# Kernel tuning notes

Measured on AMD Instinct MI355X. Metric: run time of the kernel, lower is better.

Reference implementation:

```python
import jax, jax.numpy as jnp
import numpy as np

# Mamba config (HF defaults for hidden_size=256)
VOCAB = 4096
H = 256          # hidden_size
I = 512          # intermediate_size = 2*H
N = 16           # state_size
R = 16           # time_step_rank = ceil(H/16)
K = 4            # conv_kernel
NUM_LAYERS = 4
B, L = 4, 1024
EPS = 1e-5


def _rmsnorm(x, w):
    return x * jax.lax.rsqrt(jnp.mean(x * x, axis=-1, keepdims=True) + EPS) * w


def setup_inputs() -> dict:
    key = jax.random.key(0)
    ks = jax.random.split(key, 20)
    s = 0.02
    Lyr = NUM_LAYERS
    inp = {
        'input_ids': jax.random.randint(ks[0], (B, L), 0, VOCAB),
        'lengths': jax.random.randint(ks[1], (B,), 1, L + 1),
        'embed': jax.random.normal(ks[2], (VOCAB, H)) * s,
        'norm_w': jnp.ones((Lyr, H)),
        'in_proj_w': jax.random.normal(ks[3], (Lyr, 2 * I, H)) * s,
        'conv_w': jax.random.normal(ks[4], (Lyr, I, K)) * s,
        'conv_b': jnp.zeros((Lyr, I)),
        'x_proj_w': jax.random.normal(ks[5], (Lyr, R + 2 * N, I)) * s,
        'dt_proj_w': jax.random.normal(ks[6], (Lyr, I, R)) * s,
        'dt_proj_b': jax.random.normal(ks[7], (Lyr, I)) * 0.5 - 4.0,
        'A_log': jnp.log(jnp.broadcast_to(jnp.arange(1, N + 1, dtype=jnp.float32), (Lyr, I, N))),
        'D': jnp.ones((Lyr, I)),
        'out_proj_w': jax.random.normal(ks[8], (Lyr, H, I)) * s,
        'final_norm_w': jnp.ones((H,)),
        'head_w1': jax.random.normal(ks[9], (H // 4, H)) * s,
        'head_b1': jnp.zeros((H // 4,)),
        'head_w2': jax.random.normal(ks[10], (1, H // 4)) * s,
        'head_b2': jnp.zeros((1,)),
    }
    return inp


def _mixer(x, in_proj_w, conv_w, conv_b, x_proj_w, dt_proj_w, dt_proj_b, A_log, D_, out_proj_w):
    b, l, _ = x.shape
    proj = x @ in_proj_w.T                      # (b,l,2I)
    xs, gate = proj[..., :I], proj[..., I:]
    # depthwise causal conv1d (kernel K, left pad K-1)
    xp = jnp.pad(xs, ((0, 0), (K - 1, 0), (0, 0)))
    conv = sum(xp[:, k:k + l, :] * conv_w[:, k] for k in range(K))
    xs = jax.nn.silu(conv + conv_b)             # (b,l,I)
    ssm = xs @ x_proj_w.T                       # (b,l,R+2N)
    dt_r, Bmat, Cmat = ssm[..., :R], ssm[..., R:R + N], ssm[..., R + N:]
    dt = jax.nn.softplus(dt_r @ dt_proj_w.T + dt_proj_b)   # (b,l,I)
    A = -jnp.exp(A_log)                         # (I,N)
    dA = jnp.exp(dt[..., None] * A)             # (b,l,I,N)
    dBu = (dt * xs)[..., None] * Bmat[:, :, None, :]        # (b,l,I,N)

    def step(state, inputs):
        a_t, bu_t, c_t = inputs                 # (b,I,N),(b,I,N),(b,N)
        state = a_t * state + bu_t
        y = jnp.einsum('bdn,bn->bd', state, c_t)
        return state, y

    state0 = jnp.zeros((b, I, N), dtype=x.dtype)
    _, ys = jax.lax.scan(step, state0, (dA.transpose(1, 0, 2, 3),
                                        dBu.transpose(1, 0, 2, 3),
                                        Cmat.transpose(1, 0, 2)))
    ys = ys.transpose(1, 0, 2)                  # (b,l,I)
    y = (ys + xs * D_) * jax.nn.silu(gate)
    return y @ out_proj_w.T                     # (b,l,H)


def reference(input_ids, lengths, embed, norm_w, in_proj_w, conv_w, conv_b,
              x_proj_w, dt_proj_w, dt_proj_b, A_log, D, out_proj_w,
              final_norm_w, head_w1, head_b1, head_w2, head_b2):
    h = embed[input_ids]                        # (B,L,H)
    for i in range(NUM_LAYERS):
        res = h
        x = _rmsnorm(h, norm_w[i])
        h = res + _mixer(x, in_proj_w[i], conv_w[i], conv_b[i], x_proj_w[i],
                         dt_proj_w[i], dt_proj_b[i], A_log[i], D[i], out_proj_w[i])
    h = _rmsnorm(h, final_norm_w)
    pooled = h[jnp.arange(h.shape[0]), lengths - 1]         # (B,H)
    hd = jax.nn.gelu(pooled @ head_w1.T + head_b1, approximate=False)
    out = hd @ head_w2.T + head_b2
    return out.squeeze(-1)                      # (B,)
```

## Files before the change

### kernel.cpp

```cpp
#include <hip/hip_runtime.h>
#include <hip/hip_bf16.h>

#define HDIM 256
#define IDIM 512
#define NST 16
#define KCONV 4
#define LAYERS 4
#define BATCH 4
#define LSEQ 1024
#define TOK (BATCH * LSEQ)

typedef unsigned short u16;
typedef float f32x4 __attribute__((ext_vector_type(4)));
typedef short bf16x8 __attribute__((ext_vector_type(8)));

static __device__ __forceinline__ u16 f2bf(float f) {
    __hip_bfloat16 h = __float2bfloat16(f);
    return reinterpret_cast<u16&>(h);
}
static __device__ __forceinline__ float bf2f(u16 b) {
    return __builtin_bit_cast(float, (unsigned)b << 16);
}
static __device__ __forceinline__ float bfup(uint2 u, int j) {
    unsigned w = (j < 2) ? u.x : u.y;
    unsigned bits = (j & 1) ? (w & 0xffff0000u) : (w << 16);
    return __builtin_bit_cast(float, bits);
}

#define DPP_ROW_ADD(p, CTRL)                                                   \
    p += __builtin_bit_cast(float, __builtin_amdgcn_update_dpp(                \
             0, __builtin_bit_cast(int, p), CTRL, 0xf, 0xf, false))

__global__ __launch_bounds__(256) void embed_kernel(const int* __restrict__ ids,
                                                    const float* __restrict__ embed,
                                                    float* __restrict__ h) {
    int idx = blockIdx.x * 256 + threadIdx.x;
    if (idx < TOK * HDIM) {
        int tok = idx >> 8;
        int c = idx & (HDIM - 1);
        h[idx] = embed[ids[tok] * HDIM + c];
    }
}

__global__ __launch_bounds__(256) void cvt4_bf16_kernel(const float* __restrict__ s0, u16* __restrict__ d0,
                                                        const float* __restrict__ s1, u16* __restrict__ d1,
                                                        const float* __restrict__ s2, u16* __restrict__ d2,
                                                        const float* __restrict__ s3, u16* __restrict__ d3) {
    const float* in;
    u16* out;
    int base;
    int bid = blockIdx.x;
    if (bid < 1024)      { in = s0; out = d0; base = bid; }
    else if (bid < 1536) { in = s1; out = d1; base = bid - 1024; }
    else if (bid < 1632) { in = s2; out = d2; base = bid - 1536; }
    else                 { in = s3; out = d3; base = bid - 1632; }
    int j = (base * 256 + threadIdx.x) * 4;
    float4 v = *(const float4*)&in[j];
    unsigned lo = (unsigned)f2bf(v.x) | ((unsigned)f2bf(v.y) << 16);
    unsigned hi = (unsigned)f2bf(v.z) | ((unsigned)f2bf(v.w) << 16);
    *(uint2*)&out[j] = make_uint2(lo, hi);
}

__global__ __launch_bounds__(256) void rmsnorm_kernel(const float* __restrict__ h,
                                                      const float* __restrict__ w,
                                                      u16* __restrict__ xb) {
    int wid = threadIdx.x >> 6, lane = threadIdx.x & 63;
    int tok = blockIdx.x * 4 + wid;
    float4 v = *(const float4*)&h[(size_t)tok * HDIM + lane * 4];
    float s = v.x * v.x + v.y * v.y + v.z * v.z + v.w * v.w;
    #pragma unroll
    for (int m = 32; m >= 1; m >>= 1) s += __shfl_xor(s, m, 64);
    float rstd = rsqrtf(s * (1.0f / HDIM) + 1e-5f);
    float4 wv = *(const float4*)&w[lane * 4];
    unsigned lo = (unsigned)f2bf(v.x * rstd * wv.x) | ((unsigned)f2bf(v.y * rstd * wv.y) << 16);
    unsigned hi = (unsigned)f2bf(v.z * rstd * wv.z) | ((unsigned)f2bf(v.w * rstd * wv.w) << 16);
    *(uint2*)&xb[(size_t)tok * HDIM + lane * 4] = make_uint2(lo, hi);
}

__global__ __launch_bounds__(256) void gemm_bf16_kernel(const u16* __restrict__ A,
                                                        const u16* __restrict__ W,
                                                        u16* __restrict__ C,
                                                        int M, int N, int K) {
    const int BM = 128, BK = 32;
    __shared__ __align__(16) u16 Al[BM][BK + 8];
    __shared__ __align__(16) u16 Bl[BM][BK + 8];
    int m0 = blockIdx.y * BM, n0 = blockIdx.x * BM;
    int tid = threadIdx.x;
    int lane = tid & 63;
    int wid = tid >> 6;
    int wr = wid >> 1, wc = wid & 1;
    int r = lane & 15, g = lane >> 4;

    f32x4 acc[4][4] = {};

    int srow = tid & 127;
    const u16* src = (tid < 128) ? (A + (size_t)(m0 + srow) * K)
                                 : (W + (size_t)(n0 + srow) * K);
    u16* dstrow = (tid < 128) ? &Al[srow][0] : &Bl[srow][0];

    for (int k0 = 0; k0 < K; k0 += BK) {
        uint4 v0 = *(const uint4*)(src + k0);
        uint4 v1 = *(const uint4*)(src + k0 + 8);
        uint4 v2 = *(const uint4*)(src + k0 + 16);
        uint4 v3 = *(const uint4*)(src + k0 + 24);
        __syncthreads();
        *(uint4*)(dstrow)      = v0;
        *(uint4*)(dstrow + 8)  = v1;
        *(uint4*)(dstrow + 16) = v2;
        *(uint4*)(dstrow + 24) = v3;
        __syncthreads();

        bf16x8 af[4], bfr[4];
        #pragma unroll
        for (int f = 0; f < 4; ++f) {
            af[f]  = *(const bf16x8*)&Al[wr * 64 + f * 16 + r][g * 8];
            bfr[f] = *(const bf16x8*)&Bl[wc * 64 + f * 16 + r][g * 8];
        }
        #pragma unroll
        for (int fm = 0; fm < 4; ++fm)
            #pragma unroll
            for (int fn = 0; fn < 4; ++fn)
                acc[fm][fn] = __builtin_amdgcn_mfma_f32_16x16x32_bf16(
                    af[fm], bfr[fn], acc[fm][fn], 0, 0, 0);
    }

    #pragma unroll
    for (int fm = 0; fm < 4; ++fm) {
        #pragma unroll
        for (int fn = 0; fn < 4; ++fn) {
            int col = n0 + wc * 64 + fn * 16 + r;
            #pragma unroll
            for (int v = 0; v < 4; ++v) {
                int row = m0 + wr * 64 + fm * 16 + g * 4 + v;
                C[(size_t)row * N + col] = f2bf(acc[fm][fn][v]);
            }
        }
    }
}

__global__ __launch_bounds__(256) void outproj_norm_kernel(const u16* __restrict__ Y,
                                                           const u16* __restrict__ W,
                                                           const float* __restrict__ nw,
                                                           float* __restrict__ h,
                                                           u16* __restrict__ xb) {
    __shared__ float sH[16][260];
    int m0 = blockIdx.x * 16;
    int tid = threadIdx.x;
    int lane = tid & 63;
    int w = tid >> 6;
    int r = lane & 15, g = lane >> 4;

    f32x4 acc[4] = {};
    const u16* yrow  = Y + (size_t)(m0 + r) * 512 + g * 8;
    const u16* wbase = W + (size_t)(w * 64 + r) * 512 + g * 8;
    #pragma unroll
    for (int k0 = 0; k0 < 512; k0 += 32) {
        bf16x8 af = *(const bf16x8*)(yrow + k0);
        #pragma unroll
        for (int fn = 0; fn < 4; ++fn) {
            bf16x8 bfr = *(const bf16x8*)(wbase + (size_t)fn * 16 * 512 + k0);
            acc[fn] = __builtin_amdgcn_mfma_f32_16x16x32_bf16(af, bfr, acc[fn], 0, 0, 0);
        }
    }

    #pragma unroll
    for (int fn = 0; fn < 4; ++fn) {
        int col = w * 64 + fn * 16 + r;
        #pragma unroll
        for (int v = 0; v < 4; ++v) {
            int row = g * 4 + v;
            size_t off = (size_t)(m0 + row) * HDIM + col;
            float hv = h[off] + acc[fn][v];
            h[off] = hv;
            sH[row][col] = hv;
        }
    }
    __syncthreads();

    int row = tid >> 4, part = tid & 15;
    const float* sr = &sH[row][part * 16];
    float s = 0.f;
    #pragma unroll
    for (int j = 0; j < 16; ++j) s = fmaf(sr[j], sr[j], s);
    DPP_ROW_ADD(s, 0xB1);
    DPP_ROW_ADD(s, 0x4E);
    DPP_ROW_ADD(s, 0x141);
    DPP_ROW_ADD(s, 0x140);
    float rstd = rsqrtf(s * (1.0f / HDIM) + 1e-5f);
    const float* nwp = &nw[part * 16];
    unsigned pk[8];
    #pragma unroll
    for (int j = 0; j < 8; ++j) {
        u16 lo = f2bf(sr[2 * j]     * rstd * nwp[2 * j]);
        u16 hi = f2bf(sr[2 * j + 1] * rstd * nwp[2 * j + 1]);
        pk[j] = (unsigned)lo | ((unsigned)hi << 16);
    }
    u16* dst = xb + (size_t)(m0 + row) * HDIM + part * 16;
    *(uint4*)(dst)     = make_uint4(pk[0], pk[1], pk[2], pk[3]);
    *(uint4*)(dst + 8) = make_uint4(pk[4], pk[5], pk[6], pk[7]);
}

__global__ __launch_bounds__(512) void xproj_kernel(const u16* __restrict__ proj,
                                                    const float* __restrict__ cw,
                                                    const float* __restrict__ cb,
                                                    const u16* __restrict__ W,
                                                    const u16* __restrict__ dtw,
                                                    const float* __restrict__ dtb,
                                                    float* __restrict__ bc,
                                                    float* __restrict__ dtT,
                                                    u16* __restrict__ xs_T,
                                                    u16* __restrict__ gate_T) {
    __shared__ __align__(16) u16 xsL[16][520];
    __shared__ float sP[8][16][52];
    __shared__ float sT[16][52];
    int m0 = blockIdx.x * 16;
    int tid = threadIdx.x;
    int lane = tid & 63;
    int w = tid >> 6;
    int r = lane & 15, g = lane >> 4;
    int tl = m0 & (LSEQ - 1);

    {
        int ic = tid;
        const u16* pxs = proj + (size_t)m0 * 1024 + ic;
        float4 wq = *(const float4*)&cw[ic * 4];
        float bias = cb[ic];
        float a0 = (tl >= 3) ? bf2f(pxs[-3 * 1024]) : 0.f;
        float a1 = (tl >= 2) ? bf2f(pxs[-2 * 1024]) : 0.f;
        float a2 = (tl >= 1) ? bf2f(pxs[-1 * 1024]) : 0.f;
        unsigned xr[8], gr[8];
        #pragma unroll
        for (int t = 0; t < 16; ++t) {
            float a3 = bf2f(pxs[t * 1024]);
            float acc = bias;
            acc = fmaf(a0, wq.x, acc);
            acc = fmaf(a1, wq.y, acc);
            acc = fmaf(a2, wq.z, acc);
            acc = fmaf(a3, wq.w, acc);
            float xsv = acc / (1.f + __expf(-acc));
            u16 xb16 = f2bf(xsv);
            xsL[t][ic] = xb16;
            float gv = bf2f(pxs[t * 1024 + 512]);
            gv = gv / (1.f + __expf(-gv));
            u16 gb16 = f2bf(gv);
            if (t & 1) { xr[t >> 1] |= (unsigned)xb16 << 16; gr[t >> 1] |= (unsigned)gb16 << 16; }
            else       { xr[t >> 1] = xb16;                   gr[t >> 1] = gb16; }
            a0 = a1; a1 = a2; a2 = a3;
        }
        size_t trow = (size_t)ic * TOK + m0;
        *(uint4*)&xs_T[trow]       = make_uint4(xr[0], xr[1], xr[2], xr[3]);
        *(uint4*)&xs_T[trow + 8]   = make_uint4(xr[4], xr[5], xr[6], xr[7]);
        *(uint4*)&gate_T[trow]     = make_uint4(gr[0], gr[1], gr[2], gr[3]);
        *(uint4*)&gate_T[trow + 8] = make_uint4(gr[4], gr[5], gr[6], gr[7]);
    }
    __syncthreads();

    {
        f32x4 acc[3] = {};
        const u16* wbase = W + (size_t)r * 512 + w * 64 + g * 8;
        #pragma unroll
        for (int ks = 0; ks < 2; ++ks) {
            bf16x8 af = *(const bf16x8*)&xsL[r][w * 64 + ks * 32 + g * 8];
            #pragma unroll
            for (int fn = 0; fn < 3; ++fn) {
                bf16x8 bfr = *(const bf16x8*)(wbase + (size_t)fn * 16 * 512 + ks * 32);
                acc[fn] = __builtin_amdgcn_mfma_f32_16x16x32_bf16(af, bfr, acc[fn], 0, 0, 0);
            }
        }
        #pragma unroll
        for (int fn = 0; fn < 3; ++fn)
            #pragma unroll
            for (int v = 0; v < 4; ++v)
                sP[w][g * 4 + v][fn * 16 + r] = acc[fn][v];
    }
    __syncthreads();

    #pragma unroll
    for (int e = 0; e < 2; ++e) {
        int o = tid + e * 512;
        if (o < 768) {
            int row = o / 48, col = o - row * 48;
            float s = 0.f;
            #pragma unroll
            for (int p = 0; p < 8; ++p) s += sP[p][row][col];
            sT[row][col] = s;
        }
    }
    __syncthreads();

    {
        int l = tid;
        int group = l >> 7;
        int rem = l & 127;
        int side = rem >> 6;
        int nn = (rem >> 2) & 15;
        int tq = rem & 3;
        bc[(size_t)blockIdx.x * 512 + l] = sT[group * 4 + tq][16 + side * 16 + nn];
    }

    bf16x8 bv = {};
    if (g < 2) {
        #pragma unroll
        for (int j = 0; j < 8; ++j)
            bv[j] = (short)f2bf(sT[r][g * 8 + j]);
    }
    int mbase = w * 64;
    #pragma unroll
    for (int mf = 0; mf < 4; ++mf) {
        int mrow = mbase + mf * 16;
        bf16x8 av = {};
        if (g < 2) av = *(const bf16x8*)(dtw + (size_t)(mrow + r) * 16 + g * 8);
        f32x4 a2 = __builtin_amdgcn_mfma_f32_16x16x32_bf16(av, bv, f32x4{}, 0, 0, 0);
        float4 b4 = *(const float4*)&dtb[mrow + g * 4];
        #pragma unroll
        for (int v = 0; v < 4; ++v) {
            int i = mrow + g * 4 + v;
            float val = a2[v] + (&b4.x)[v];
            val = fmaxf(val, 0.f) + log1pf(__expf(-fabsf(val)));
            dtT[(size_t)i * TOK + m0 + r] = val;
        }
    }
}

__global__ __launch_bounds__(256) void scan_kernel(const float* __restrict__ dt_T,
                                                   const u16* __restrict__ xs_T,
                                                   const u16* __restrict__ gate_T,
                                                   const float* __restrict__ bc,
                                                   const float* __restrict__ A_log,
                                                   const float* __restrict__ Dw,
                                                   u16* __restrict__ yb) {
    int tid = threadIdx.x;
    int w = tid >> 6;
    int lane = tid & 63;
    int nq = lane & 3;
    int c = lane >> 2;

    int lin = (blockIdx.x & 7) * 64 + (blockIdx.x >> 3);
    int base = lin * 4;
    int bi = base + w;
    int b = bi >> 9;
    int i = bi & (IDIM - 1);

    float A[4];
    #pragma unroll
    for (int k = 0; k < 4; ++k) A[k] = -__expf(A_log[i * NST + nq * 4 + k]);

    __shared__ float aprodS[4][16][16];
    __shared__ float stendS[4][16][16];
    __shared__ float incS[4][16][16];

    int t0 = c * 64;
    size_t coff = (size_t)i * TOK + b * LSEQ + t0;
    const float4* dtp = (const float4*)(dt_T + coff);
    const uint2*  xsp = (const uint2*)(xs_T + coff);
    const u16*    xg  = xs_T + coff;
    const u16*    gg  = gate_T + coff;
    const float4* bp  = (const float4*)(bc + (size_t)(b * LSEQ + t0) * 32);

    float st[4] = {0.f, 0.f, 0.f, 0.f};
    float sumdt = 0.f;
    #pragma unroll
    for (int q = 0; q < 16; ++q) {
        float4 d4 = dtp[q];
        uint2  xu = xsp[q];
        float4 Bq[4];
        #pragma unroll
        for (int k = 0; k < 4; ++k) Bq[k] = __builtin_bit_cast(float4, bp[q * 32 + nq * 4 + k]);
        #pragma unroll
        for (int j = 0; j < 4; ++j) {
            float dtv = (&d4.x)[j];
            sumdt += dtv;
            float dxv = dtv * bfup(xu, j);
            #pragma unroll
            for (int k = 0; k < 4; ++k)
                st[k] = fmaf(__expf(dtv * A[k]), st[k], dxv * (&Bq[k].x)[j]);
        }
    }
    #pragma unroll
    for (int k = 0; k < 4; ++k) {
        aprodS[w][c][nq * 4 + k] = __expf(A[k] * sumdt);
        stendS[w][c][nq * 4 + k] = st[k];
    }
    __syncthreads();

    if (tid < 64) {
        int ch = tid >> 4, n = tid & 15;
        float carry = 0.f;
        for (int cc = 0; cc < 16; ++cc) {
            incS[ch][cc][n] = carry;
            carry = fmaf(aprodS[ch][cc][n], carry, stendS[ch][cc][n]);
        }
    }
    __syncthreads();

    #pragma unroll
    for (int k = 0; k < 4; ++k) st[k] = incS[w][c][nq * 4 + k];
    float Dv = Dw[i];
    u16* y_b = yb + ((size_t)b * LSEQ + t0) * IDIM + i;

    #pragma unroll
    for (int q = 0; q < 16; ++q) {
        float4 d4 = dtp[q];
        uint2  xu = xsp[q];
        float4 Bq[4], Cq[4];
        #pragma unroll
        for (int k = 0; k < 4; ++k) {
            Bq[k] = __builtin_bit_cast(float4, bp[q * 32 + nq * 4 + k]);
            Cq[k] = __builtin_bit_cast(float4, bp[q * 32 + 16 + nq * 4 + k]);
        }
        float yacc = 0.f;
        #pragma unroll
        for (int j = 0; j < 4; ++j) {
            float dtv = (&d4.x)[j];
            float dxv = dtv * bfup(xu, j);
            float py = 0.f;
            #pragma unroll
            for (int k = 0; k < 4; ++k) {
                st[k] = fmaf(__expf(dtv * A[k]), st[k], dxv * (&Bq[k].x)[j]);
                py = fmaf(st[k], (&Cq[k].x)[j], py);
            }
            DPP_ROW_ADD(py, 0xB1);
            DPP_ROW_ADD(py, 0x4E);
            yacc = (j == nq) ? py : yacc;
        }
        int t = q * 4 + nq;
        float xvn = bf2f(xg[t]);
        float gvn = bf2f(gg[t]);
        y_b[(size_t)t * IDIM] = f2bf(fmaf(xvn, Dv, yacc) * gvn);
    }
}

__global__ __launch_bounds__(256) void head_kernel(const float* __restrict__ h,
                                                   const int* __restrict__ lengths,
                                                   const float* __restrict__ fw,
                                                   const float* __restrict__ w1,
                                                   const float* __restrict__ b1,
                                                   const float* __restrict__ w2,
                                                   const float* __restrict__ b2,
                                                   float* __restrict__ out) {
    int b = blockIdx.x;
    int c = threadIdx.x;
    int len = lengths[b];
    const float* row = h + ((size_t)b * LSEQ + (len - 1)) * HDIM;
    float v = row[c];
    float s = v * v;
    #pragma unroll
    for (int m = 32; m >= 1; m >>= 1) s += __shfl_xor(s, m, 64);
    __shared__ float ls[4];
    __shared__ float pooled[HDIM];
    __shared__ float hd[64];
    if ((c & 63) == 0) ls[c >> 6] = s;
    __syncthreads();
    float tot = ls[0] + ls[1] + ls[2] + ls[3];
    float rstd = rsqrtf(tot * (1.0f / HDIM) + 1e-5f);
    pooled[c] = v * rstd * fw[c];
    __syncthreads();
    if (c < 64) {
        float a = b1[c];
        for (int k = 0; k < HDIM; ++k) a = fmaf(pooled[k], w1[c * HDIM + k], a);
        float g = 0.5f * a * (1.f + erff(a * 0.70710678118654752f));
        hd[c] = g * w2[c];
    }
    __syncthreads();
    if (c == 0) {
        float o = b2[0];
        for (int k = 0; k < 64; ++k) o += hd[k];
        out[b] = o;
    }
}

extern "C" void kernel_launch(void* const* d_in, const int* in_sizes, int n_in,
                              void* d_out, int out_size, void* d_ws, size_t ws_size,
                              hipStream_t stream) {
    const int*   ids         = (const int*)d_in[0];
    const int*   lengths     = (const int*)d_in[1];
    const float* embed       = (const float*)d_in[2];
    const float* norm_w      = (const float*)d_in[3];
    const float* in_proj_w   = (const float*)d_in[4];
    const float* conv_w      = (const float*)d_in[5];
    const float* conv_b      = (const float*)d_in[6];
    const float* x_proj_w    = (const float*)d_in[7];
    const float* dt_proj_w   = (const float*)d_in[8];
    const float* dt_proj_b   = (const float*)d_in[9];
    const float* A_log       = (const float*)d_in[10];
    const float* Dw          = (const float*)d_in[11];
    const float* out_proj_w  = (const float*)d_in[12];
    const float* final_norm_w= (const float*)d_in[13];
    const float* head_w1     = (const float*)d_in[14];
    const float* head_b1     = (const float*)d_in[15];
    const float* head_w2     = (const float*)d_in[16];
    const float* head_b2     = (const float*)d_in[17];

    float* ws   = (float*)d_ws;
    float* h    = ws;
    float* dtT  = h    + 1048576;
    float* bc   = dtT  + 2097152;
    u16* xb   = (u16*)(bc + 131072);
    u16* yb   = xb   + 1048576;
    u16* wib  = yb   + 2097152;
    u16* wob  = wib  + 1048576;
    u16* xwb  = wob  + 524288;
    u16* dtwb = xwb  + 98304;
    u16* projb= dtwb + 32768;
    u16* xsT  = projb+ 4194304;
    u16* gT   = xsT  + 2097152;

    embed_kernel<<<TOK * HDIM / 256, 256, 0, stream>>>(ids, embed, h);
    cvt4_bf16_kernel<<<1664, 256, 0, stream>>>(in_proj_w, wib, out_proj_w, wob,
                                               x_proj_w, xwb, dt_proj_w, dtwb);
    rmsnorm_kernel<<<TOK / 4, 256, 0, stream>>>(h, norm_w, xb);

    for (int l = 0; l < LAYERS; ++l) {
        gemm_bf16_kernel<<<dim3(1024 / 128, TOK / 128), 256, 0, stream>>>(
            xb, wib + (size_t)l * 2 * IDIM * HDIM, projb, TOK, 2 * IDIM, HDIM);
        xproj_kernel<<<TOK / 16, 512, 0, stream>>>(
            projb, conv_w + l * IDIM * KCONV, conv_b + l * IDIM,
            xwb + (size_t)l * 48 * IDIM, dtwb + (size_t)l * IDIM * 16,
            dt_proj_b + l * IDIM, bc, dtT, xsT, gT);
        scan_kernel<<<BATCH * IDIM / 4, 256, 0, stream>>>(
            dtT, xsT, gT, bc, A_log + (size_t)l * IDIM * NST, Dw + l * IDIM, yb);
        const float* nw_next = (l + 1 < LAYERS) ? (norm_w + (l + 1) * HDIM) : final_norm_w;
        outproj_norm_kernel<<<TOK / 16, 256, 0, stream>>>(
            yb, wob + (size_t)l * HDIM * IDIM, nw_next, h, xb);
    }

    head_kernel<<<BATCH, 256, 0, stream>>>(h, lengths, final_norm_w,
                                           head_w1, head_b1, head_w2, head_b2,
                                           (float*)d_out);
}
```

Before: 323.4 us.

## Split scan into 64 chunks per channel with wave-shuffle carry scan

Each block now handles one (batch, channel) pair, with 64 time chunks of 16 steps instead of 16 chunks of 64 steps across 4 channels. The launch grid grows fourfold. The serial carry loop over chunks is replaced by a Hillis-Steele shuffle scan within a wavefront, and shared arrays are padded to 17 columns to avoid bank conflicts. The intent is to shorten the serial per-thread recurrence and raise parallelism, at the cost of more blocks, shorter memory streams per thread and extra scan work.

```diff
diff --git a/kernel.cpp b/kernel.cpp
--- a/kernel.cpp
+++ b/kernel.cpp
@@ -330,26 +330,22 @@
                                                    const float* __restrict__ Dw,
                                                    u16* __restrict__ yb) {
     int tid = threadIdx.x;
-    int w = tid >> 6;
-    int lane = tid & 63;
-    int nq = lane & 3;
-    int c = lane >> 2;
-
-    int lin = (blockIdx.x & 7) * 64 + (blockIdx.x >> 3);
-    int base = lin * 4;
-    int bi = base + w;
-    int b = bi >> 9;
-    int i = bi & (IDIM - 1);
+    int c  = tid >> 2;
+    int nq = tid & 3;
+
+    int lin = (blockIdx.x & 7) * 256 + (blockIdx.x >> 3);
+    int b = lin >> 9;
+    int i = lin & (IDIM - 1);
 
     float A[4];
     #pragma unroll
     for (int k = 0; k < 4; ++k) A[k] = -__expf(A_log[i * NST + nq * 4 + k]);
 
-    __shared__ float aprodS[4][16][16];
-    __shared__ float stendS[4][16][16];
-    __shared__ float incS[4][16][16];
-
-    int t0 = c * 64;
+    __shared__ float aprodS[64][17];
+    __shared__ float stendS[64][17];
+    __shared__ float incS[64][17];
+
+    int t0 = c * 16;
     size_t coff = (size_t)i * TOK + b * LSEQ + t0;
     const float4* dtp = (const float4*)(dt_T + coff);
     const uint2*  xsp = (const uint2*)(xs_T + coff);
@@ -360,7 +356,7 @@
     float st[4] = {0.f, 0.f, 0.f, 0.f};
     float sumdt = 0.f;
     #pragma unroll
-    for (int q = 0; q < 16; ++q) {
+    for (int q = 0; q < 4; ++q) {
         float4 d4 = dtp[q];
         uint2  xu = xsp[q];
         float4 Bq[4];
@@ -378,28 +374,38 @@
     }
     #pragma unroll
     for (int k = 0; k < 4; ++k) {
-        aprodS[w][c][nq * 4 + k] = __expf(A[k] * sumdt);
-        stendS[w][c][nq * 4 + k] = st[k];
-    }
-    __syncthreads();
-
-    if (tid < 64) {
-        int ch = tid >> 4, n = tid & 15;
-        float carry = 0.f;
-        for (int cc = 0; cc < 16; ++cc) {
-            incS[ch][cc][n] = carry;
-            carry = fmaf(aprodS[ch][cc][n], carry, stendS[ch][cc][n]);
-        }
-    }
-    __syncthreads();
-
-    #pragma unroll
-    for (int k = 0; k < 4; ++k) st[k] = incS[w][c][nq * 4 + k];
+        aprodS[c][nq * 4 + k] = __expf(A[k] * sumdt);
+        stendS[c][nq * 4 + k] = st[k];
+    }
+    __syncthreads();
+
+    {
+        int wv = tid >> 6;
+        int lc = tid & 63;
+        #pragma unroll
+        for (int m = 0; m < 4; ++m) {
+            int n = wv * 4 + m;
+            float a = aprodS[lc][n];
+            float s = stendS[lc][n];
+            #pragma unroll
+            for (int off = 1; off < 64; off <<= 1) {
+                float a_up = __shfl_up(a, off, 64);
+                float s_up = __shfl_up(s, off, 64);
+                if (lc >= off) { s = fmaf(a, s_up, s); a *= a_up; }
+            }
+            float inc = __shfl_up(s, 1, 64);
+            incS[lc][n] = (lc == 0) ? 0.f : inc;
+        }
+    }
+    __syncthreads();
+
+    #pragma unroll
+    for (int k = 0; k < 4; ++k) st[k] = incS[c][nq * 4 + k];
     float Dv = Dw[i];
     u16* y_b = yb + ((size_t)b * LSEQ + t0) * IDIM + i;
 
     #pragma unroll
-    for (int q = 0; q < 16; ++q) {
+    for (int q = 0; q < 4; ++q) {
         float4 d4 = dtp[q];
         uint2  xu = xsp[q];
         float4 Bq[4], Cq[4];
@@ -517,7 +523,7 @@
             projb, conv_w + l * IDIM * KCONV, conv_b + l * IDIM,
             xwb + (size_t)l * 48 * IDIM, dtwb + (size_t)l * IDIM * 16,
             dt_proj_b + l * IDIM, bc, dtT, xsT, gT);
-        scan_kernel<<<BATCH * IDIM / 4, 256, 0, stream>>>(
+        scan_kernel<<<BATCH * IDIM, 256, 0, stream>>>(
             dtT, xsT, gT, bc, A_log + (size_t)l * IDIM * NST, Dw + l * IDIM, yb);
         const float* nw_next = (l + 1 < LAYERS) ? (norm_w + (l + 1) * HDIM) : final_norm_w;
         outproj_norm_kernel<<<TOK / 16, 256, 0, stream>>>(
```

After: 337.7 us. 4.4% more time.
